# Performance work log

Hardware: AMD Instinct MI355X
Metric: run time of the kernel (lower is better)

## Reference

```python
import jax, jax.numpy as jnp
import numpy as np

N, E, H, F = 100000, 1000000, 4, 64
D_IN = 64


def _gat_conv(x, src, dst, W, al, ar, b, act):
    # x: [N, D_in], W: [D_in, H*F], al/ar: [H, F], b: [H, F]
    z = (x @ W).reshape(N, H, F)
    el = jnp.sum(z * al, axis=-1)              # [N, H]
    er = jnp.sum(z * ar, axis=-1)              # [N, H]
    e = jax.nn.leaky_relu(el[src] + er[dst], 0.2)   # [E, H]
    # edge softmax over incoming edges of each dst node
    m = jax.ops.segment_max(e, dst, num_segments=N)  # [N, H]
    ex = jnp.exp(e - m[dst])                         # [E, H]
    s = jax.ops.segment_sum(ex, dst, num_segments=N)  # [N, H]
    alpha = ex / s[dst]                              # [E, H]
    msg = z[src] * alpha[..., None]                  # [E, H, F] (largest intermediate)
    out = jax.ops.segment_sum(msg, dst, num_segments=N) + b  # [N, H, F]
    return act(out)


def setup_inputs() -> dict:
    key = jax.random.key(0)
    ks = jax.random.split(key, 12)
    sc_in = 1.0 / np.sqrt(D_IN)
    sc_f = 1.0 / np.sqrt(F)
    return {
        "x": jax.random.normal(ks[0], (N, D_IN), jnp.float32),
        "src": jax.random.randint(ks[1], (E,), 0, N, jnp.int32),
        "dst": jax.random.randint(ks[2], (E,), 0, N, jnp.int32),
        "W1": jax.random.normal(ks[3], (D_IN, H * F), jnp.float32) * sc_in,
        "al1": jax.random.normal(ks[4], (H, F), jnp.float32) * sc_f,
        "ar1": jax.random.normal(ks[5], (H, F), jnp.float32) * sc_f,
        "b1": jnp.zeros((H, F), jnp.float32),
        "W2": jax.random.normal(ks[6], (F, H * F), jnp.float32) * sc_f,
        "al2": jax.random.normal(ks[7], (H, F), jnp.float32) * sc_f,
        "ar2": jax.random.normal(ks[8], (H, F), jnp.float32) * sc_f,
        "b2": jnp.zeros((H, F), jnp.float32),
    }


def reference(x, src, dst, W1, al1, ar1, b1, W2, al2, ar2, b2):
    # layer 1: GATConv with tanh activation, then mean over heads
    h = _gat_conv(x, src, dst, W1, al1, ar1, b1, jnp.tanh)   # [N, H, F]
    h = h.mean(axis=-2)                                      # [N, F]
    # layer 2: GATConv (no activation), then mean over heads
    h = _gat_conv(h, src, dst, W2, al2, ar2, b2, lambda v: v)
    return h.mean(axis=-2)                                   # [N, F]
```

## Files before the change

kernel.cpp:

```cpp
#include <hip/hip_runtime.h>

typedef _Float16 f16x8 __attribute__((ext_vector_type(8)));
typedef _Float16 f16x4 __attribute__((ext_vector_type(4)));
typedef _Float16 f16x2 __attribute__((ext_vector_type(2)));
typedef float f32x4 __attribute__((ext_vector_type(4)));

#define PADB 16
#define MAXNB 512
#define TILE_A 4096

__device__ __forceinline__ float lrelu(float v) { return v >= 0.f ? v : 0.2f * v; }
__device__ __forceinline__ float cexp(float v) { return __expf(fminf(v, 60.f)); }
__device__ __forceinline__ float ftanh(float x) {
    float e = __expf(fminf(2.f * x, 30.f));
    return (e - 1.f) / (e + 1.f);
}

__global__ __launch_bounds__(256) void k_wprep(
    const float* __restrict__ W1, const float* __restrict__ al1, const float* __restrict__ ar1,
    const float* __restrict__ W2, const float* __restrict__ al2, const float* __restrict__ ar2,
    float* __restrict__ A1l, float* __restrict__ A1r,
    float* __restrict__ A2l, float* __restrict__ A2r,
    _Float16* __restrict__ Wt1, _Float16* __restrict__ Wt2,
    int* __restrict__ bktc, int nb)
{
    int b = blockIdx.x, t = threadIdx.x;
    if (b < 2) {
        const float* W  = b ? W2 : W1;
        const float* al = b ? al2 : al1;
        const float* ar = b ? ar2 : ar1;
        float* Al = b ? A2l : A1l;
        float* Ar = b ? A2r : A1r;
        _Float16* Wt = b ? Wt2 : Wt1;
        int k = t >> 2, h = t & 3;
        float sl = 0.f, sr = 0.f;
#pragma unroll 8
        for (int f = 0; f < 64; ++f) {
            float wv = W[k * 256 + h * 64 + f];
            sl = fmaf(wv, al[h * 64 + f], sl);
            sr = fmaf(wv, ar[h * 64 + f], sr);
        }
        Al[k * 4 + h] = sl;
        Ar[k * 4 + h] = sr;
        int col = t;
#pragma unroll 8
        for (int kk = 0; kk < 64; ++kk)
            Wt[col * 64 + kk] = (_Float16)W[kk * 256 + col];
    } else {
        for (int i = t; i < nb; i += 256) bktc[(size_t)i * PADB] = 0;
    }
}

__global__ __launch_bounds__(256) void k_elr_hist(
    const float* __restrict__ Xf, _Float16* __restrict__ XhOut,
    const float* __restrict__ Al, const float* __restrict__ Ar,
    float* __restrict__ el, float* __restrict__ er, int nNodes,
    const int* __restrict__ dst, int* __restrict__ bktc, int E_, int ebBlocks,
    int nb)
{
    int b = blockIdx.x;
    if (b < ebBlocks) {
        __shared__ int lb[MAXNB];
        int t = threadIdx.x;
        for (int i = t; i < nb; i += 256) lb[i] = 0;
        __syncthreads();
        int base = b * TILE_A;
        int end = base + TILE_A; if (end > E_) end = E_;
        for (int j = base + t; j < end; j += 256)
            atomicAdd(&lb[((unsigned)dst[j]) >> 8], 1);
        __syncthreads();
        for (int i = t; i < nb; i += 256) {
            int c = lb[i];
            if (c) atomicAdd(&bktc[(size_t)i * PADB], c);
        }
        return;
    }
    int lane = threadIdx.x & 63, wid = threadIdx.x >> 6;
    int q = lane >> 4, c = lane & 15;
    int n = (b - ebBlocks) * 16 + wid * 4 + q;
    if (n >= nNodes) return;
    float4 xv = *reinterpret_cast<const float4*>(Xf + (size_t)n * 64 + c * 4);
    f16x4 xh4 = {(_Float16)xv.x, (_Float16)xv.y, (_Float16)xv.z, (_Float16)xv.w};
    *reinterpret_cast<f16x4*>(XhOut + (size_t)n * 64 + c * 4) = xh4;
    float p0 = 0.f, p1 = 0.f, p2 = 0.f, p3 = 0.f;
    float q0 = 0.f, q1 = 0.f, q2 = 0.f, q3 = 0.f;
    float xs[4] = {xv.x, xv.y, xv.z, xv.w};
#pragma unroll
    for (int i = 0; i < 4; ++i) {
        float4 av = *reinterpret_cast<const float4*>(Al + (c * 4 + i) * 4);
        float4 rv = *reinterpret_cast<const float4*>(Ar + (c * 4 + i) * 4);
        p0 = fmaf(xs[i], av.x, p0); p1 = fmaf(xs[i], av.y, p1);
        p2 = fmaf(xs[i], av.z, p2); p3 = fmaf(xs[i], av.w, p3);
        q0 = fmaf(xs[i], rv.x, q0); q1 = fmaf(xs[i], rv.y, q1);
        q2 = fmaf(xs[i], rv.z, q2); q3 = fmaf(xs[i], rv.w, q3);
    }
#pragma unroll
    for (int m = 1; m <= 8; m <<= 1) {
        p0 += __shfl_xor(p0, m, 64); p1 += __shfl_xor(p1, m, 64);
        p2 += __shfl_xor(p2, m, 64); p3 += __shfl_xor(p3, m, 64);
        q0 += __shfl_xor(q0, m, 64); q1 += __shfl_xor(q1, m, 64);
        q2 += __shfl_xor(q2, m, 64); q3 += __shfl_xor(q3, m, 64);
    }
    if (c == 0) {
        *reinterpret_cast<float4*>(el + (size_t)n * 4) = make_float4(p0, p1, p2, p3);
        *reinterpret_cast<float4*>(er + (size_t)n * 4) = make_float4(q0, q1, q2, q3);
    }
}

__global__ __launch_bounds__(256) void k_elr2(
    const _Float16* __restrict__ Xh,
    const float* __restrict__ Al, const float* __restrict__ Ar,
    float* __restrict__ el, float* __restrict__ er, int nNodes)
{
    int lane = threadIdx.x & 63, wid = threadIdx.x >> 6;
    int q = lane >> 4, c = lane & 15;
    int n = blockIdx.x * 16 + wid * 4 + q;
    if (n >= nNodes) return;
    f16x4 xh4 = *reinterpret_cast<const f16x4*>(Xh + (size_t)n * 64 + c * 4);
    float p0 = 0.f, p1 = 0.f, p2 = 0.f, p3 = 0.f;
    float q0 = 0.f, q1 = 0.f, q2 = 0.f, q3 = 0.f;
#pragma unroll
    for (int i = 0; i < 4; ++i) {
        float xs = (float)xh4[i];
        float4 av = *reinterpret_cast<const float4*>(Al + (c * 4 + i) * 4);
        float4 rv = *reinterpret_cast<const float4*>(Ar + (c * 4 + i) * 4);
        p0 = fmaf(xs, av.x, p0); p1 = fmaf(xs, av.y, p1);
        p2 = fmaf(xs, av.z, p2); p3 = fmaf(xs, av.w, p3);
        q0 = fmaf(xs, rv.x, q0); q1 = fmaf(xs, rv.y, q1);
        q2 = fmaf(xs, rv.z, q2); q3 = fmaf(xs, rv.w, q3);
    }
#pragma unroll
    for (int m = 1; m <= 8; m <<= 1) {
        p0 += __shfl_xor(p0, m, 64); p1 += __shfl_xor(p1, m, 64);
        p2 += __shfl_xor(p2, m, 64); p3 += __shfl_xor(p3, m, 64);
        q0 += __shfl_xor(q0, m, 64); q1 += __shfl_xor(q1, m, 64);
        q2 += __shfl_xor(q2, m, 64); q3 += __shfl_xor(q3, m, 64);
    }
    if (c == 0) {
        *reinterpret_cast<float4*>(el + (size_t)n * 4) = make_float4(p0, p1, p2, p3);
        *reinterpret_cast<float4*>(er + (size_t)n * 4) = make_float4(q0, q1, q2, q3);
    }
}

__global__ void k_bscan(const int* __restrict__ bktc, int* __restrict__ bbase,
                        int* __restrict__ bcur, int nb) {
    int lane = threadIdx.x;
    int carry = 0;
    for (int base = 0; base < nb; base += 64) {
        int i = base + lane;
        int v = (i < nb) ? bktc[(size_t)i * PADB] : 0;
        int sc = v;
#pragma unroll
        for (int d = 1; d < 64; d <<= 1) {
            int u = __shfl_up(sc, d, 64);
            if (lane >= d) sc += u;
        }
        if (i < nb) {
            int ex = carry + sc - v;
            bbase[i] = ex;
            bcur[(size_t)i * PADB] = ex;
        }
        carry += __shfl(sc, 63, 64);
    }
    if (lane == 0) bbase[nb] = carry;
}

__global__ __launch_bounds__(256) void k_binA(
    const int* __restrict__ src, const int* __restrict__ dst,
    int* __restrict__ bcur, unsigned* __restrict__ ebkt, int E_, int nb)
{
    __shared__ int lcnt[MAXNB];
    __shared__ int lcur[MAXNB];
    __shared__ int lofs[MAXNB];
    __shared__ int gbase[MAXNB];
    __shared__ unsigned spack[TILE_A];
    __shared__ int gposs[TILE_A];
    int t = threadIdx.x;
    int tile0 = blockIdx.x * TILE_A;
    int cntT = E_ - tile0; if (cntT > TILE_A) cntT = TILE_A;

    for (int i = t; i < nb; i += 256) { lcnt[i] = 0; lcur[i] = 0; }
    __syncthreads();

    int myS[16], myD[16];
#pragma unroll
    for (int k = 0; k < 16; ++k) {
        int idx = k * 256 + t;
        if (idx < cntT) {
            myS[k] = src[tile0 + idx];
            myD[k] = dst[tile0 + idx];
            atomicAdd(&lcnt[((unsigned)myD[k]) >> 8], 1);
        }
    }
    __syncthreads();

    for (int i = t; i < nb; i += 256) {
        int c = lcnt[i];
        gbase[i] = c ? atomicAdd(&bcur[(size_t)i * PADB], c) : 0;
    }
    if (t < 64) {
        int carry = 0;
        for (int base = 0; base < nb; base += 64) {
            int i = base + t;
            int v = (i < nb) ? lcnt[i] : 0;
            int sc = v;
#pragma unroll
            for (int d = 1; d < 64; d <<= 1) {
                int u = __shfl_up(sc, d, 64);
                if (t >= d) sc += u;
            }
            if (i < nb) lofs[i] = carry + sc - v;
            carry += __shfl(sc, 63, 64);
        }
    }
    __syncthreads();

#pragma unroll
    for (int k = 0; k < 16; ++k) {
        int idx = k * 256 + t;
        if (idx < cntT) {
            int b = ((unsigned)myD[k]) >> 8;
            int slot = atomicAdd(&lcur[b], 1);
            int lidx = lofs[b] + slot;
            spack[lidx] = (unsigned)myS[k] | (((unsigned)myD[k] & 255u) << 17);
            gposs[lidx] = gbase[b] + slot;
        }
    }
    __syncthreads();

    for (int j = t; j < cntT; j += 256)
        ebkt[gposs[j]] = spack[j];
}

__global__ __launch_bounds__(256) void k_binC(
    const unsigned* __restrict__ ebkt, const int* __restrict__ bbase,
    int* __restrict__ cnt, int nNodes)
{
    __shared__ int lc[256];
    int b = blockIdx.x, t = threadIdx.x;
    lc[t] = 0;
    __syncthreads();
    int s0 = bbase[b], s1 = bbase[b + 1];
    for (int j = s0 + t; j < s1; j += 256)
        atomicAdd(&lc[ebkt[j] >> 17], 1);
    __syncthreads();
    int node = (b << 8) + t;
    if (node < nNodes) cnt[node] = lc[t];
}

__global__ __launch_bounds__(256) void k_binB(
    const unsigned* __restrict__ ebkt, const int* __restrict__ bbase,
    const int* __restrict__ offs, int* __restrict__ esrc, int nNodes)
{
    __shared__ int lcur[256];
    __shared__ int lofs[256];
    int b = blockIdx.x, t = threadIdx.x;
    lcur[t] = 0;
    int node = (b << 8) + t;
    lofs[t] = (node < nNodes) ? offs[node] : 0;
    __syncthreads();
    int s0 = bbase[b], s1 = bbase[b + 1];
    for (int j = s0 + t; j < s1; j += 256) {
        unsigned v = ebkt[j];
        int dl = v >> 17;
        int p = lofs[dl] + atomicAdd(&lcur[dl], 1);
        esrc[p] = (int)(v & 0x1FFFFu);
    }
}

#define SC_VPT 8
#define SC_CHUNK 2048

__global__ __launch_bounds__(256) void k_chunk_sums(const int* __restrict__ cnt,
                                                    int* __restrict__ bsums, int n) {
    int tid = threadIdx.x;
    int base = blockIdx.x * SC_CHUNK + tid * SC_VPT;
    int s = 0;
#pragma unroll
    for (int i = 0; i < SC_VPT; ++i) { int idx = base + i; if (idx < n) s += cnt[idx]; }
#pragma unroll
    for (int m = 1; m < 64; m <<= 1) s += __shfl_xor(s, m, 64);
    int lane = tid & 63, wid = tid >> 6;
    __shared__ int sh[4];
    if (lane == 0) sh[wid] = s;
    __syncthreads();
    if (tid == 0) bsums[blockIdx.x] = sh[0] + sh[1] + sh[2] + sh[3];
}

__global__ void k_scan_mid(int* bsums, int nb) {
    int lane = threadIdx.x & 63;
    int carry = 0;
    for (int base = 0; base < nb; base += 64) {
        int i = base + lane;
        int v = (i < nb) ? bsums[i] : 0;
        int sc = v;
#pragma unroll
        for (int d = 1; d < 64; d <<= 1) {
            int t = __shfl_up(sc, d, 64);
            if (lane >= d) sc += t;
        }
        if (i < nb) bsums[i] = carry + sc - v;
        carry += __shfl(sc, 63, 64);
    }
}

__global__ __launch_bounds__(256) void k_scan_write(const int* __restrict__ cnt,
                                                    const int* __restrict__ bsums,
                                                    int* __restrict__ offs, int n) {
    int tid = threadIdx.x;
    int base = blockIdx.x * SC_CHUNK + tid * SC_VPT;
    int v[SC_VPT]; int s = 0;
#pragma unroll
    for (int i = 0; i < SC_VPT; ++i) { int idx = base + i; v[i] = (idx < n) ? cnt[idx] : 0; s += v[i]; }
    int lane = tid & 63, wid = tid >> 6;
    int sc = s;
#pragma unroll
    for (int d = 1; d < 64; d <<= 1) { int t = __shfl_up(sc, d, 64); if (lane >= d) sc += t; }
    __shared__ int wsum[4];
    if (lane == 63) wsum[wid] = sc;
    __syncthreads();
    int wbase = 0;
    for (int i = 0; i < wid; ++i) wbase += wsum[i];
    int p = bsums[blockIdx.x] + wbase + (sc - s);
#pragma unroll
    for (int i = 0; i < SC_VPT; ++i) {
        int idx = base + i;
        if (idx < n) {
            offs[idx] = p; p += v[i];
            if (idx == n - 1) offs[n] = p;
        }
    }
}

#define SGP_LOAD(rr, XV) { \
    _Pragma("unroll") for (int u_ = 0; u_ < 4; ++u_) { \
        int e_ = sidx[nl][4 * (rr) + u_]; \
        XV[u_] = *reinterpret_cast<const f16x4*>(Xh + (size_t)(unsigned)e_ * 64 + c4); } }

#define SGP_FMA(rr, XV) { \
    int2 aw_[4]; \
    _Pragma("unroll") for (int u_ = 0; u_ < 4; ++u_) aw_[u_] = salp[nl][4 * (rr) + u_]; \
    _Pragma("unroll") for (int u_ = 0; u_ < 4; ++u_) { \
        f16x2 wa_ = __builtin_bit_cast(f16x2, aw_[u_].x); \
        f16x2 wb_ = __builtin_bit_cast(f16x2, aw_[u_].y); \
        _Pragma("unroll") for (int i_ = 0; i_ < 4; ++i_) { \
            float xf_ = (float)XV[u_][i_]; \
            A0[i_] = fmaf((float)wa_[0], xf_, A0[i_]); \
            A1[i_] = fmaf((float)wa_[1], xf_, A1[i_]); \
            A2[i_] = fmaf((float)wb_[0], xf_, A2[i_]); \
            A3[i_] = fmaf((float)wb_[1], xf_, A3[i_]); } } }

template <typename OutT>
__global__ __launch_bounds__(256, 4) void k_sgp(
    const int* __restrict__ esrc, const int* __restrict__ offs,
    const float* __restrict__ el, const float* __restrict__ er,
    const _Float16* __restrict__ Xh,
    const _Float16* __restrict__ Wt, const float* __restrict__ B,
    OutT* __restrict__ out, int nNodes, int do_tanh)
{
    __shared__ _Float16 sagg[16 * 264];
    __shared__ int  sidx[16][17];
    __shared__ int2 salp[16][17];
    int tid = threadIdx.x;
    int lane = tid & 63, wid = tid >> 6;
    int q = lane >> 4, c = lane & 15, c4 = c * 4;
    int n = blockIdx.x * 16 + wid * 4 + q;
    int nl = wid * 4 + q;
    bool valid = n < nNodes;

    float A0[4] = {}, A1[4] = {}, A2[4] = {}, A3[4] = {};
    if (valid) {
        int s0 = offs[n], s1 = offs[n + 1];
        int d = s1 - s0;
        int dc = d > 16 ? 16 : d;
        int R = (dc + 3) >> 2;
        float4 erv = *reinterpret_cast<const float4*>(er + (size_t)n * 4);
        bool has = c < d;

        int sreg = has ? esrc[s0 + c] : 0;
        sidx[nl][c] = sreg;
        float4 v = has ? *reinterpret_cast<const float4*>(el + (size_t)sreg * 4)
                       : make_float4(0.f, 0.f, 0.f, 0.f);
        f16x4 xva[4], xvb[4];
        if (R > 0) SGP_LOAD(0, xva);
        if (R > 1) SGP_LOAD(1, xvb);

        float x0 = 0.f, x1 = 0.f, x2 = 0.f, x3 = 0.f;
        if (has) {
            x0 = cexp(lrelu(v.x + erv.x)); x1 = cexp(lrelu(v.y + erv.y));
            x2 = cexp(lrelu(v.z + erv.z)); x3 = cexp(lrelu(v.w + erv.w));
        }
        float t0 = x0, t1 = x1, t2 = x2, t3 = x3;
        for (int j = s0 + c + 16; j < s1; j += 16) {
            int s = esrc[j];
            float4 w = *reinterpret_cast<const float4*>(el + (size_t)s * 4);
            t0 += cexp(lrelu(w.x + erv.x)); t1 += cexp(lrelu(w.y + erv.y));
            t2 += cexp(lrelu(w.z + erv.z)); t3 += cexp(lrelu(w.w + erv.w));
        }
#pragma unroll
        for (int m = 1; m <= 8; m <<= 1) {
            t0 += __shfl_xor(t0, m, 64); t1 += __shfl_xor(t1, m, 64);
            t2 += __shfl_xor(t2, m, 64); t3 += __shfl_xor(t3, m, 64);
        }
        float i0 = 1.f / t0, i1 = 1.f / t1, i2 = 1.f / t2, i3 = 1.f / t3;

        int2 ap = make_int2(0, 0);
        if (has) {
            f16x2 pa = {(_Float16)(x0 * i0), (_Float16)(x1 * i1)};
            f16x2 pb = {(_Float16)(x2 * i2), (_Float16)(x3 * i3)};
            ap.x = __builtin_bit_cast(int, pa);
            ap.y = __builtin_bit_cast(int, pb);
        }
        salp[nl][c] = ap;

        if (R > 0) { SGP_FMA(0, xva); if (R > 2) SGP_LOAD(2, xva); }
        if (R > 1) { SGP_FMA(1, xvb); if (R > 3) SGP_LOAD(3, xvb); }
        if (R > 2) SGP_FMA(2, xva);
        if (R > 3) SGP_FMA(3, xvb);

        for (int base = s0 + 16; base < s1; base += 16) {
            int cnt_ = s1 - base; if (cnt_ > 16) cnt_ = 16;
            int sj = 0; int2 a2 = make_int2(0, 0);
            if (c < cnt_) {
                sj = esrc[base + c];
                float4 w = *reinterpret_cast<const float4*>(el + (size_t)sj * 4);
                f16x2 pa = {(_Float16)(cexp(lrelu(w.x + erv.x)) * i0),
                            (_Float16)(cexp(lrelu(w.y + erv.y)) * i1)};
                f16x2 pb = {(_Float16)(cexp(lrelu(w.z + erv.z)) * i2),
                            (_Float16)(cexp(lrelu(w.w + erv.w)) * i3)};
                a2.x = __builtin_bit_cast(int, pa);
                a2.y = __builtin_bit_cast(int, pb);
            }
            sidx[nl][c] = sj;
            salp[nl][c] = a2;
            int rnd = (cnt_ + 3) >> 2;
            for (int r = 0; r < rnd; ++r) {
                f16x4 xr[4];
                SGP_LOAD(r, xr);
                SGP_FMA(r, xr);
            }
        }
    }
    {
        _Float16* aggr = sagg + nl * 264;
        f16x4 h0, h1v, h2, h3;
#pragma unroll
        for (int i = 0; i < 4; ++i) {
            h0[i] = (_Float16)A0[i]; h1v[i] = (_Float16)A1[i];
            h2[i] = (_Float16)A2[i]; h3[i] = (_Float16)A3[i];
        }
        *reinterpret_cast<f16x4*>(aggr + c4)       = h0;
        *reinterpret_cast<f16x4*>(aggr + 64 + c4)  = h1v;
        *reinterpret_cast<f16x4*>(aggr + 128 + c4) = h2;
        *reinterpret_cast<f16x4*>(aggr + 192 + c4) = h3;
    }

    int col = c, quad = q, f0 = wid * 16;
    f16x8 bfrag[4][2];
    float bias[4];
#pragma unroll
    for (int h = 0; h < 4; ++h) {
#pragma unroll
        for (int ks = 0; ks < 2; ++ks)
            bfrag[h][ks] = *reinterpret_cast<const f16x8*>(
                Wt + (h * 64 + f0 + col) * 64 + ks * 32 + quad * 8);
        bias[h] = B[h * 64 + f0 + col];
    }
    __syncthreads();

    const _Float16* ap = sagg + col * 264 + quad * 8;
    f32x4 acc = {0.f, 0.f, 0.f, 0.f};
#pragma unroll
    for (int h = 0; h < 4; ++h) {
        f16x8 a0 = *reinterpret_cast<const f16x8*>(ap + h * 64);
        f16x8 a1 = *reinterpret_cast<const f16x8*>(ap + h * 64 + 32);
        f32x4 dd = {0.f, 0.f, 0.f, 0.f};
        dd = __builtin_amdgcn_mfma_f32_16x16x32_f16(a0, bfrag[h][0], dd, 0, 0, 0);
        dd = __builtin_amdgcn_mfma_f32_16x16x32_f16(a1, bfrag[h][1], dd, 0, 0, 0);
        if (do_tanh) {
#pragma unroll
            for (int r = 0; r < 4; ++r) acc[r] += ftanh(dd[r] + bias[h]);
        } else {
#pragma unroll
            for (int r = 0; r < 4; ++r) acc[r] += dd[r] + bias[h];
        }
    }
    int n0 = blockIdx.x * 16;
#pragma unroll
    for (int r = 0; r < 4; ++r) {
        int row = n0 + quad * 4 + r;
        if (row < nNodes)
            out[(size_t)row * 64 + f0 + col] = (OutT)(0.25f * acc[r]);
    }
}

extern "C" void kernel_launch(void* const* d_in, const int* in_sizes, int n_in,
                              void* d_out, int out_size, void* d_ws, size_t ws_size,
                              hipStream_t stream) {
    const float* x   = (const float*)d_in[0];
    const int*   src = (const int*)d_in[1];
    const int*   dst = (const int*)d_in[2];
    const float* W1  = (const float*)d_in[3];
    const float* al1 = (const float*)d_in[4];
    const float* ar1 = (const float*)d_in[5];
    const float* b1  = (const float*)d_in[6];
    const float* W2  = (const float*)d_in[7];
    const float* al2 = (const float*)d_in[8];
    const float* ar2 = (const float*)d_in[9];
    const float* b2  = (const float*)d_in[10];
    float* out = (float*)d_out;

    int N_ = in_sizes[0] / 64;
    int E_ = in_sizes[1];
    int NB_ = (N_ + 255) >> 8;

    char* ws = (char*)d_ws;
    size_t off = 0;
    auto alloc = [&](size_t bytes) -> void* {
        void* p = ws + off;
        off = (off + bytes + 255) & ~(size_t)255;
        return p;
    };
    _Float16* xh  = (_Float16*)alloc(((size_t)N_ + 16) * 64 * 2);
    _Float16* h1h = (_Float16*)alloc(((size_t)N_ + 16) * 64 * 2);
    float* el   = (float*)alloc(((size_t)N_ + 16) * 4 * 4);
    float* er   = (float*)alloc(((size_t)N_ + 16) * 4 * 4);
    int*   cnt  = (int*)alloc((size_t)(N_ + 16) * 4);
    int*   offs = (int*)alloc((size_t)(N_ + 1) * 4);
    int*   esrc = (int*)alloc((size_t)E_ * 4);
    unsigned* ebkt = (unsigned*)alloc((size_t)E_ * 4);
    int*   bktc = (int*)alloc((size_t)MAXNB * PADB * 4);
    int*   bcur = (int*)alloc((size_t)MAXNB * PADB * 4);
    int*   bbase= (int*)alloc((size_t)(MAXNB + 1) * 4);
    int*   bsums= (int*)alloc(4096);
    float* A1l  = (float*)alloc(64 * 4 * 4);
    float* A1r  = (float*)alloc(64 * 4 * 4);
    float* A2l  = (float*)alloc(64 * 4 * 4);
    float* A2r  = (float*)alloc(64 * 4 * 4);
    _Float16* Wt1 = (_Float16*)alloc(256 * 64 * 2);
    _Float16* Wt2 = (_Float16*)alloc(256 * 64 * 2);

    k_wprep<<<3, 256, 0, stream>>>(W1, al1, ar1, W2, al2, ar2,
                                   A1l, A1r, A2l, A2r, Wt1, Wt2, bktc, NB_);

    int hb = (E_ + TILE_A - 1) / TILE_A;
    int nb16 = (N_ + 15) / 16;
    k_elr_hist<<<hb + nb16, 256, 0, stream>>>(x, xh, A1l, A1r, el, er, N_,
                                              dst, bktc, E_, hb, NB_);
    k_bscan<<<1, 64, 0, stream>>>(bktc, bbase, bcur, NB_);
    k_binA<<<hb, 256, 0, stream>>>(src, dst, bcur, ebkt, E_, NB_);
    k_binC<<<NB_, 256, 0, stream>>>(ebkt, bbase, cnt, N_);
    int nchunks = (N_ + SC_CHUNK - 1) / SC_CHUNK;
    k_chunk_sums<<<nchunks, 256, 0, stream>>>(cnt, bsums, N_);
    k_scan_mid<<<1, 64, 0, stream>>>(bsums, nchunks);
    k_scan_write<<<nchunks, 256, 0, stream>>>(cnt, bsums, offs, N_);
    k_binB<<<NB_, 256, 0, stream>>>(ebkt, bbase, offs, esrc, N_);

    k_sgp<_Float16><<<nb16, 256, 0, stream>>>(esrc, offs, el, er, xh,
                                              Wt1, b1, h1h, N_, 1);
    k_elr2<<<nb16, 256, 0, stream>>>(h1h, A2l, A2r, el, er, N_);
    k_sgp<float><<<nb16, 256, 0, stream>>>(esrc, offs, el, er, h1h,
                                           Wt2, b2, out, N_, 0);
}
```

Measured before the change: 274.5 us.

## Fuse per-node count, offset scan and scatter into one bucket kernel

```diff
diff --git a/kernel.cpp b/kernel.cpp
--- a/kernel.cpp
+++ b/kernel.cpp
@@ -143,7 +143,8 @@
 }
 
 __global__ void k_bscan(const int* __restrict__ bktc, int* __restrict__ bbase,
-                        int* __restrict__ bcur, int nb) {
+                        int* __restrict__ bcur, int* __restrict__ offs,
+                        int nb, int nNodes) {
     int lane = threadIdx.x;
     int carry = 0;
     for (int base = 0; base < nb; base += 64) {
@@ -162,7 +163,7 @@
         }
         carry += __shfl(sc, 63, 64);
     }
-    if (lane == 0) bbase[nb] = carry;
+    if (lane == 0) { bbase[nb] = carry; offs[nNodes] = carry; }
 }
 
 __global__ __launch_bounds__(256) void k_binA(
@@ -232,11 +233,13 @@
         ebkt[gposs[j]] = spack[j];
 }
 
-__global__ __launch_bounds__(256) void k_binC(
+__global__ __launch_bounds__(256) void k_bin2(
     const unsigned* __restrict__ ebkt, const int* __restrict__ bbase,
-    int* __restrict__ cnt, int nNodes)
+    int* __restrict__ offs, int* __restrict__ esrc, int nNodes)
 {
     __shared__ int lc[256];
+    __shared__ int lofs[256];
+    __shared__ int wsum[4];
     int b = blockIdx.x, t = threadIdx.x;
     lc[t] = 0;
     __syncthreads();
@@ -244,91 +247,26 @@
     for (int j = s0 + t; j < s1; j += 256)
         atomicAdd(&lc[ebkt[j] >> 17], 1);
     __syncthreads();
-    int node = (b << 8) + t;
-    if (node < nNodes) cnt[node] = lc[t];
-}
-
-__global__ __launch_bounds__(256) void k_binB(
-    const unsigned* __restrict__ ebkt, const int* __restrict__ bbase,
-    const int* __restrict__ offs, int* __restrict__ esrc, int nNodes)
-{
-    __shared__ int lcur[256];
-    __shared__ int lofs[256];
-    int b = blockIdx.x, t = threadIdx.x;
-    lcur[t] = 0;
-    int node = (b << 8) + t;
-    lofs[t] = (node < nNodes) ? offs[node] : 0;
-    __syncthreads();
-    int s0 = bbase[b], s1 = bbase[b + 1];
-    for (int j = s0 + t; j < s1; j += 256) {
-        unsigned v = ebkt[j];
-        int dl = v >> 17;
-        int p = lofs[dl] + atomicAdd(&lcur[dl], 1);
-        esrc[p] = (int)(v & 0x1FFFFu);
-    }
-}
-
-#define SC_VPT 8
-#define SC_CHUNK 2048
-
-__global__ __launch_bounds__(256) void k_chunk_sums(const int* __restrict__ cnt,
-                                                    int* __restrict__ bsums, int n) {
-    int tid = threadIdx.x;
-    int base = blockIdx.x * SC_CHUNK + tid * SC_VPT;
-    int s = 0;
-#pragma unroll
-    for (int i = 0; i < SC_VPT; ++i) { int idx = base + i; if (idx < n) s += cnt[idx]; }
-#pragma unroll
-    for (int m = 1; m < 64; m <<= 1) s += __shfl_xor(s, m, 64);
-    int lane = tid & 63, wid = tid >> 6;
-    __shared__ int sh[4];
-    if (lane == 0) sh[wid] = s;
-    __syncthreads();
-    if (tid == 0) bsums[blockIdx.x] = sh[0] + sh[1] + sh[2] + sh[3];
-}
-
-__global__ void k_scan_mid(int* bsums, int nb) {
-    int lane = threadIdx.x & 63;
-    int carry = 0;
-    for (int base = 0; base < nb; base += 64) {
-        int i = base + lane;
-        int v = (i < nb) ? bsums[i] : 0;
-        int sc = v;
-#pragma unroll
-        for (int d = 1; d < 64; d <<= 1) {
-            int t = __shfl_up(sc, d, 64);
-            if (lane >= d) sc += t;
-        }
-        if (i < nb) bsums[i] = carry + sc - v;
-        carry += __shfl(sc, 63, 64);
-    }
-}
-
-__global__ __launch_bounds__(256) void k_scan_write(const int* __restrict__ cnt,
-                                                    const int* __restrict__ bsums,
-                                                    int* __restrict__ offs, int n) {
-    int tid = threadIdx.x;
-    int base = blockIdx.x * SC_CHUNK + tid * SC_VPT;
-    int v[SC_VPT]; int s = 0;
-#pragma unroll
-    for (int i = 0; i < SC_VPT; ++i) { int idx = base + i; v[i] = (idx < n) ? cnt[idx] : 0; s += v[i]; }
-    int lane = tid & 63, wid = tid >> 6;
-    int sc = s;
-#pragma unroll
-    for (int d = 1; d < 64; d <<= 1) { int t = __shfl_up(sc, d, 64); if (lane >= d) sc += t; }
-    __shared__ int wsum[4];
+    int v = lc[t];
+    int lane = t & 63, wid = t >> 6;
+    int sc = v;
+#pragma unroll
+    for (int d = 1; d < 64; d <<= 1) { int u = __shfl_up(sc, d, 64); if (lane >= d) sc += u; }
     if (lane == 63) wsum[wid] = sc;
     __syncthreads();
     int wbase = 0;
     for (int i = 0; i < wid; ++i) wbase += wsum[i];
-    int p = bsums[blockIdx.x] + wbase + (sc - s);
-#pragma unroll
-    for (int i = 0; i < SC_VPT; ++i) {
-        int idx = base + i;
-        if (idx < n) {
-            offs[idx] = p; p += v[i];
-            if (idx == n - 1) offs[n] = p;
-        }
+    int ex = s0 + wbase + (sc - v);
+    lofs[t] = ex;
+    int node = (b << 8) + t;
+    if (node < nNodes) offs[node] = ex;
+    lc[t] = 0;
+    __syncthreads();
+    for (int j = s0 + t; j < s1; j += 256) {
+        unsigned e = ebkt[j];
+        int dl = e >> 17;
+        int p = lofs[dl] + atomicAdd(&lc[dl], 1);
+        esrc[p] = (int)(e & 0x1FFFFu);
     }
 }
 
@@ -525,14 +463,12 @@
     _Float16* h1h = (_Float16*)alloc(((size_t)N_ + 16) * 64 * 2);
     float* el   = (float*)alloc(((size_t)N_ + 16) * 4 * 4);
     float* er   = (float*)alloc(((size_t)N_ + 16) * 4 * 4);
-    int*   cnt  = (int*)alloc((size_t)(N_ + 16) * 4);
     int*   offs = (int*)alloc((size_t)(N_ + 1) * 4);
     int*   esrc = (int*)alloc((size_t)E_ * 4);
     unsigned* ebkt = (unsigned*)alloc((size_t)E_ * 4);
     int*   bktc = (int*)alloc((size_t)MAXNB * PADB * 4);
     int*   bcur = (int*)alloc((size_t)MAXNB * PADB * 4);
     int*   bbase= (int*)alloc((size_t)(MAXNB + 1) * 4);
-    int*   bsums= (int*)alloc(4096);
     float* A1l  = (float*)alloc(64 * 4 * 4);
     float* A1r  = (float*)alloc(64 * 4 * 4);
     float* A2l  = (float*)alloc(64 * 4 * 4);
@@ -547,14 +483,9 @@
     int nb16 = (N_ + 15) / 16;
     k_elr_hist<<<hb + nb16, 256, 0, stream>>>(x, xh, A1l, A1r, el, er, N_,
                                               dst, bktc, E_, hb, NB_);
-    k_bscan<<<1, 64, 0, stream>>>(bktc, bbase, bcur, NB_);
+    k_bscan<<<1, 64, 0, stream>>>(bktc, bbase, bcur, offs, NB_, N_);
     k_binA<<<hb, 256, 0, stream>>>(src, dst, bcur, ebkt, E_, NB_);
-    k_binC<<<NB_, 256, 0, stream>>>(ebkt, bbase, cnt, N_);
-    int nchunks = (N_ + SC_CHUNK - 1) / SC_CHUNK;
-    k_chunk_sums<<<nchunks, 256, 0, stream>>>(cnt, bsums, N_);
-    k_scan_mid<<<1, 64, 0, stream>>>(bsums, nchunks);
-    k_scan_write<<<nchunks, 256, 0, stream>>>(cnt, bsums, offs, N_);
-    k_binB<<<NB_, 256, 0, stream>>>(ebkt, bbase, offs, esrc, N_);
+    k_bin2<<<NB_, 256, 0, stream>>>(ebkt, bbase, offs, esrc, N_);
 
     k_sgp<_Float16><<<nb16, 256, 0, stream>>>(esrc, offs, el, er, xh,
                                               Wt1, b1, h1h, N_, 1);
```

New measurement: 265.2 us. 1.04x faster.
